# Optimization experiments

Measured on AMD Instinct MI355X. Metric: run time of the kernel, lower is better.

The kernel has to match this reference:

```python
import jax, jax.numpy as jnp
import numpy as np

B, T, C, J = 2048, 128, 3, 25   # batch, frames, coords, joints
E = 64                          # structure elements (n_elements)


def setup_inputs() -> dict:
    key = jax.random.key(0)
    k1, k2 = jax.random.split(key)
    x = jax.random.normal(k1, (B, T, C, J), dtype=jnp.float32)
    centres = jax.random.uniform(k2, (E, 2), dtype=jnp.float32)
    sharpness = jnp.full((E, 2), 3.0, dtype=jnp.float32)  # torch init: ones*3
    return {"x": x, "centres": centres, "sharpness": sharpness}


def _mst_deaths(Dm):
    """Prim's MST over dense distance matrix Dm [n,n].
    The multiset of MST edge weights equals the finite death times of the
    0-dim Vietoris-Rips persistence diagram (births are all 0)."""
    n = Dm.shape[0]
    in_tree0 = jnp.zeros(n, dtype=bool).at[0].set(True)

    def step(carry, _):
        mind, in_tree = carry
        masked = jnp.where(in_tree, jnp.inf, mind)  # distance from tree to each node
        j = jnp.argmin(masked)
        w = masked[j]                               # weight of edge added to MST
        in_tree = in_tree.at[j].set(True)
        mind = jnp.minimum(mind, Dm[j])
        return (mind, in_tree), w

    (_, _), deaths = jax.lax.scan(step, (Dm[0], in_tree0), None, length=n - 1)
    return deaths  # [n-1]


def reference(x, centres, sharpness):
    # --- dense preprocessing ---
    h = x.mean(1)                           # [B, C, J]
    h = h[..., :, None] - h[..., None, :]   # [B, C, J, J] pairwise coord diffs
    h = h.mean(-3)                          # [B, J, J]
    h = jnp.sqrt((h * h).sum(axis=1))       # torch.norm(., 2, dim=1) -> [B, J]
    lo, hi = h.min(), h.max()
    rng = hi - lo
    safe = rng > 1e-8
    h = jnp.where(safe, (h - lo) / jnp.where(safe, rng, 1.0), jnp.zeros_like(h))

    # --- Vietoris-Rips dim-0 persistence on point cloud h: B points in J dims ---
    sq = (h * h).sum(-1)
    d2 = sq[:, None] + sq[None, :] - 2.0 * (h @ h.T)       # [B, B]
    Dm = jnp.sqrt(jnp.maximum(d2, 1e-12))
    deaths = _mst_deaths(Dm)                               # [B-1]
    pd = jnp.stack([jnp.zeros_like(deaths), deaths], -1)[None]  # [1, P, 2]

    # --- StructureElementLayer: out[b,e] = sum_p exp(-sum_d s[e,d]^2 (pd-c)^2) ---
    s2 = sharpness * sharpness                             # [E, 2]
    diff = pd[:, :, None, :] - centres[None, None, :, :]   # [1, P, E, 2]
    out = jnp.exp(-(diff * diff * s2).sum(-1)).sum(1)      # [1, E]
    return out
```

## Files before the change

kernel.cpp:

```cpp
#include <hip/hip_runtime.h>
#include <math.h>

#define B_N 2048
#define T_N 128
#define C_N 3
#define J_N 25
#define E_N 64
#define TC  (T_N*C_N)
#define TCJ (TC*J_N)
#define NQ4 (TCJ/4)

#define D_OFF      0
#define H_OFF      (B_N*B_N)
#define BLO_OFF    (H_OFF + B_N*J_N)
#define BHI_OFF    (BLO_OFF + B_N)
#define DEATHS_OFF (BHI_OFF + B_N)
#define BEST_OFF   (DEATHS_OFF + B_N)
#define COMP_OFF   (BEST_OFF + 4*B_N)
#define GC_OFF     (COMP_OFF + 2*B_N)
#define DC_OFF     (GC_OFF + 2)

typedef unsigned long long u64;
#define U64MAX 0xFFFFFFFFFFFFFFFFull
#define U32INF 0xFFFFFFFFu

__global__ void __launch_bounds__(256) k_reduce(const float* __restrict__ x,
                                                float* __restrict__ ws) {
    __shared__ float4 part[250];
    __shared__ float S[100];
    __shared__ float Mj[25];
    const int t = threadIdx.x, b = blockIdx.x;
    const float4* x4 = (const float4*)(x + (size_t)b * TCJ);
    if (t < 250) {
        float4 a; a.x = a.y = a.z = a.w = 0.f;
        for (int idx = t; idx < NQ4; idx += 250) {
            float4 v = x4[idx];
            a.x += v.x; a.y += v.y; a.z += v.z; a.w += v.w;
        }
        part[t] = a;
    }
    __syncthreads();
    if (t < 25) {
        float4 s = part[t];
        #pragma unroll
        for (int g = 1; g < 10; ++g) {
            float4 v = part[t + 25 * g];
            s.x += v.x; s.y += v.y; s.z += v.z; s.w += v.w;
        }
        S[4*t] = s.x; S[4*t+1] = s.y; S[4*t+2] = s.z; S[4*t+3] = s.w;
    }
    __syncthreads();
    if (t < 25) Mj[t] = (S[t] + S[t+25] + S[t+50] + S[t+75]) * (1.0f / 384.0f);
    __syncthreads();
    if (t < 25) {
        float mj = Mj[t], acc = 0.f;
        #pragma unroll
        for (int i = 0; i < J_N; ++i) { float d = Mj[i] - mj; acc += d * d; }
        float hv = sqrtf(acc);
        ws[H_OFF + b * J_N + t] = hv;
        S[t] = hv;
    }
    __syncthreads();
    if (t == 0) {
        float lo = S[0], hi = S[0];
        #pragma unroll
        for (int i = 1; i < J_N; ++i) { lo = fminf(lo, S[i]); hi = fmaxf(hi, S[i]); }
        ws[BLO_OFF + b] = lo;
        ws[BHI_OFF + b] = hi;
    }
}

__global__ void k_dist(float* ws) {
    __shared__ float A[16][26], Bsh[16][26];
    const int tx = threadIdx.x, ty = threadIdx.y;
    const int flat = ty * 16 + tx;
    const int rowA = blockIdx.x * 16, rowB = blockIdx.y * 16;
    const float* h = ws + H_OFF;
    for (int idx = flat; idx < 16 * J_N; idx += 256) {
        int r = idx / J_N, c = idx % J_N;
        A[r][c]   = h[(rowA + r) * J_N + c];
        Bsh[r][c] = h[(rowB + r) * J_N + c];
    }
    __syncthreads();
    float acc = 0.f;
    #pragma unroll
    for (int k = 0; k < J_N; ++k) {
        float d = A[ty][k] - Bsh[tx][k];
        acc += d * d;
    }
    float* D = ws + D_OFF;
    D[(size_t)(rowA + ty) * B_N + rowB + tx] = sqrtf(fmaxf(acc, 1e-12f));
}

__global__ void __launch_bounds__(1024) k_scan0(float* __restrict__ ws) {
    const int t = threadIdx.x, w = t >> 6, lane = t & 63;
    const int row = blockIdx.x * 16 + w;
    const float4* row4 = (const float4*)(ws + D_OFF + (size_t)row * B_N);
    u64 best = U64MAX;
    #pragma unroll
    for (int k = 0; k < 8; ++k) {
        const int q = k * 64 + lane;
        float4 w4 = row4[q];
        const unsigned j0 = (unsigned)(q * 4);
        float wv[4] = {w4.x, w4.y, w4.z, w4.w};
        #pragma unroll
        for (int m = 0; m < 4; ++m) {
            unsigned j = j0 + m;
            if (j != (unsigned)row) {
                unsigned a = min((unsigned)row, j), b2 = max((unsigned)row, j);
                u64 key = ((u64)__float_as_uint(wv[m]) << 32) | (a << 11) | b2;
                if (key < best) best = key;
            }
        }
    }
    #pragma unroll
    for (int off = 32; off; off >>= 1) {
        u64 o = __shfl_down(best, off);
        if (o < best) best = o;
    }
    if (lane == 0) ((u64*)(ws + BEST_OFF))[row] = best;
    if (blockIdx.x == 0) {
        unsigned* gc = (unsigned*)(ws + COMP_OFF);
        gc[t] = (unsigned)t; gc[t + 1024] = (unsigned)(t + 1024);
        unsigned* dc = (unsigned*)(ws + DC_OFF);
        #pragma unroll
        for (int i = 0; i < 4; ++i) dc[i * 1024 + t] = U32INF;
        if (t == 0) { ((unsigned*)(ws + GC_OFF))[0] = 0u; ((unsigned*)(ws + GC_OFF))[1] = 0u; }
    }
}

__global__ void __launch_bounds__(1024) k_round(float* __restrict__ ws, int par_in,
                                                int do_scan) {
    unsigned* gcnt = (unsigned*)(ws + GC_OFF);
    const unsigned base = gcnt[par_in];
    if (base >= B_N - 1) return;
    __shared__ __align__(16) unsigned comp[B_N];
    __shared__ u64 cb[B_N];
    __shared__ unsigned par[B_N];
    __shared__ unsigned cnt_s;
    const int t = threadIdx.x, blk = blockIdx.x;
    const unsigned* gcomp_in = (const unsigned*)(ws + COMP_OFF) + par_in * B_N;
    unsigned* gcomp_out = (unsigned*)(ws + COMP_OFF) + (par_in ^ 1) * B_N;
    const u64* bin = (const u64*)(ws + BEST_OFF) + par_in * B_N;
    u64* bout = (u64*)(ws + BEST_OFF) + (par_in ^ 1) * B_N;
    float* deaths = ws + DEATHS_OFF;

    if (t == 0) cnt_s = 0u;
    comp[t] = gcomp_in[t]; comp[t + 1024] = gcomp_in[t + 1024];
    cb[t] = U64MAX; cb[t + 1024] = U64MAX;
    __syncthreads();
    #pragma unroll
    for (int i = t; i < B_N; i += 1024) {
        u64 bk = bin[i];
        if (bk != U64MAX) atomicMin(&cb[comp[i]], bk);
    }
    __syncthreads();
    #pragma unroll
    for (int c = t; c < B_N; c += 1024) {
        u64 k = cb[c];
        unsigned p = (unsigned)c;
        if (k != U64MAX) {
            unsigned a  = (unsigned)((k >> 11) & 0x7FFu);
            unsigned b2 = (unsigned)(k & 0x7FFu);
            unsigned ca = comp[a], cbv = comp[b2];
            unsigned c2 = (ca == (unsigned)c) ? cbv : ca;
            p = c2;
            if (!(cb[c2] == k && c2 < (unsigned)c)) {
                unsigned li = atomicAdd(&cnt_s, 1u);
                if (blk == 0) deaths[base + li] = __uint_as_float((unsigned)(k >> 32));
            }
        }
        par[c] = p;
    }
    __syncthreads();
    #pragma unroll
    for (int c = t; c < B_N; c += 1024) {
        unsigned p = par[c];
        if (p != (unsigned)c && par[p] == (unsigned)c && (unsigned)c < p) par[c] = (unsigned)c;
    }
    __syncthreads();
    #pragma unroll
    for (int c = t; c < B_N; c += 1024) {
        unsigned r = par[c];
        while (true) { unsigned pr = par[r]; if (pr == r) break; r = pr; }
        par[c] = r;
    }
    __syncthreads();
    #pragma unroll
    for (int i = t; i < B_N; i += 1024) comp[i] = par[comp[i]];
    __syncthreads();
    const unsigned newbase = base + cnt_s;
    if (blk == 0) {
        gcomp_out[t] = comp[t]; gcomp_out[t + 1024] = comp[t + 1024];
        if (t == 0) { gcnt[par_in ^ 1] = newbase; if (newbase >= B_N - 1) gcnt[par_in] = newbase; }
    }
    if (!do_scan || newbase >= B_N - 1) return;

    const int w = t >> 6, lane = t & 63;
    const int row = blk * 16 + w;
    const unsigned ci = comp[row];
    u64 prev = bin[row];
    {
        unsigned pa = (unsigned)((prev >> 11) & 0x7FFu);
        unsigned pb = (unsigned)(prev & 0x7FFu);
        unsigned jo = (pa == (unsigned)row) ? pb : pa;
        if (comp[jo] != ci) {
            if (lane == 0) bout[row] = prev;
            return;
        }
    }
    const float4* row4 = (const float4*)(ws + D_OFF + (size_t)row * B_N);
    const uint4* comp4 = (const uint4*)comp;
    u64 best = U64MAX;
    #pragma unroll
    for (int k = 0; k < 8; ++k) {
        const int q = k * 64 + lane;
        float4 w4 = row4[q];
        uint4  c4 = comp4[q];
        const unsigned j0 = (unsigned)(q * 4);
        float wv[4] = {w4.x, w4.y, w4.z, w4.w};
        unsigned cv[4] = {c4.x, c4.y, c4.z, c4.w};
        #pragma unroll
        for (int m = 0; m < 4; ++m) {
            if (cv[m] != ci) {
                unsigned j = j0 + m;
                unsigned a = min((unsigned)row, j), b2 = max((unsigned)row, j);
                u64 key = ((u64)__float_as_uint(wv[m]) << 32) | (a << 11) | b2;
                if (key < best) best = key;
            }
        }
    }
    #pragma unroll
    for (int off = 32; off; off >>= 1) {
        u64 o = __shfl_down(best, off);
        if (o < best) best = o;
    }
    if (lane == 0) bout[row] = best;
}

__global__ void __launch_bounds__(1024) k_contract(float* __restrict__ ws) {
    if (((const unsigned*)(ws + GC_OFF))[1] >= B_N - 1) return;
    __shared__ unsigned cflag[B_N];
    __shared__ unsigned Dcs[64 * 64];
    __shared__ unsigned csum[16];
    const int t = threadIdx.x, blk = blockIdx.x;
    const unsigned lane = t & 63, w = t >> 6;
    const unsigned* gcomp1 = (const unsigned*)(ws + COMP_OFF) + B_N;

    cflag[t] = 0u; cflag[t + 1024] = 0u;
    #pragma unroll
    for (int i = 0; i < 4; ++i) Dcs[i * 1024 + t] = U32INF;
    __syncthreads();
    unsigned cA = gcomp1[t], cB = gcomp1[t + 1024];
    cflag[cA] = 1u; cflag[cB] = 1u;
    __syncthreads();
    unsigned f0 = cflag[2 * t], f1 = cflag[2 * t + 1];
    unsigned s = f0 + f1, sc = s;
    #pragma unroll
    for (int off = 1; off < 64; off <<= 1) {
        unsigned v = __shfl_up(sc, off);
        if (lane >= (unsigned)off) sc += v;
    }
    if (lane == 63) csum[w] = sc;
    __syncthreads();
    if (t < 16) {
        unsigned v = csum[t], acc = v;
        #pragma unroll
        for (int off = 1; off < 16; off <<= 1) {
            unsigned u2 = __shfl_up(acc, off);
            if (t >= off) acc += u2;
        }
        csum[t] = acc - v;
    }
    __syncthreads();
    unsigned off0 = csum[w] + (sc - s);
    __syncthreads();
    if (f0) cflag[2 * t] = off0;
    if (f1) cflag[2 * t + 1] = off0 + f0;
    __syncthreads();

    #pragma unroll
    for (int q2 = 0; q2 < 2; ++q2) {
        const int row = blk * 32 + (int)w * 2 + q2;
        const unsigned ci = gcomp1[row];
        const unsigned ri = cflag[ci];
        const float4* row4 = (const float4*)(ws + D_OFF + (size_t)row * B_N);
        const uint4* comp4 = (const uint4*)gcomp1;
        #pragma unroll
        for (int k = 0; k < 8; ++k) {
            const int q = k * 64 + (int)lane;
            float4 w4 = row4[q];
            uint4  c4 = comp4[q];
            float wv[4] = {w4.x, w4.y, w4.z, w4.w};
            unsigned cv[4] = {c4.x, c4.y, c4.z, c4.w};
            #pragma unroll
            for (int m = 0; m < 4; ++m) {
                if (cv[m] != ci) {
                    unsigned rj = cflag[cv[m]];
                    atomicMin(&Dcs[ri * 64 + rj], __float_as_uint(wv[m]));
                }
            }
        }
    }
    __syncthreads();
    unsigned* gDc = (unsigned*)(ws + DC_OFF);
    #pragma unroll
    for (int i = t; i < 4096; i += 1024) {
        unsigned v = Dcs[i];
        if (v != U32INF) atomicMin(&gDc[i], v);
    }
}

__global__ void __launch_bounds__(1024) k_finishstruct(float* __restrict__ ws,
                                                       const float* __restrict__ centres,
                                                       const float* __restrict__ sharp,
                                                       float* __restrict__ out) {
    __shared__ unsigned Dcs[64 * 64];
    __shared__ u64 cbf[64];
    __shared__ unsigned parf[64], ccomp[64];
    __shared__ unsigned cnt_s, base_s;
    __shared__ float redlo[16], redhi[16];
    const int t = threadIdx.x;
    const unsigned lane = t & 63, w = t >> 6;
    float* deaths = ws + DEATHS_OFF;
    const unsigned base0 = ((const unsigned*)(ws + GC_OFF))[1];

    if (base0 < B_N - 1) {
        const unsigned* gDc = (const unsigned*)(ws + DC_OFF);
        #pragma unroll
        for (int i = 0; i < 4; ++i) Dcs[i * 1024 + t] = gDc[i * 1024 + t];
        if (t < 64) ccomp[t] = (unsigned)t;
        if (t == 0) base_s = base0;
        __syncthreads();
        for (int iter = 0; iter < 7; ++iter) {
            if (t < 64) cbf[t] = U64MAX;
            if (t == 0) cnt_s = 0u;
            __syncthreads();
            #pragma unroll
            for (int q2 = 0; q2 < 4; ++q2) {
                const int r = (int)w * 4 + q2;
                const unsigned cc = ccomp[r];
                unsigned wv = Dcs[r * 64 + lane];
                u64 key = U64MAX;
                if (wv != U32INF && ccomp[lane] != cc) {
                    unsigned a = min((unsigned)r, lane), b2 = max((unsigned)r, lane);
                    key = ((u64)wv << 32) | (a << 6) | b2;
                }
                #pragma unroll
                for (int off = 32; off; off >>= 1) {
                    u64 o = __shfl_down(key, off);
                    if (o < key) key = o;
                }
                if (lane == 0 && key != U64MAX) atomicMin(&cbf[cc], key);
            }
            __syncthreads();
            if (w == 0) {
                u64 k = cbf[lane];
                unsigned p = lane;
                bool add = false; float dw = 0.f;
                if (k != U64MAX) {
                    unsigned a = (unsigned)((k >> 6) & 63u), b2 = (unsigned)(k & 63u);
                    unsigned ca = ccomp[a], cbv = ccomp[b2];
                    unsigned c2 = (ca == lane) ? cbv : ca;
                    p = c2;
                    if (!(cbf[c2] == k && c2 < lane)) {
                        add = true; dw = __uint_as_float((unsigned)(k >> 32));
                    }
                }
                parf[lane] = p;
                unsigned pp = parf[lane];
                if (pp != lane && parf[pp] == lane && lane < pp) parf[lane] = lane;
                unsigned r2 = parf[lane];
                while (parf[r2] != r2) r2 = parf[r2];
                parf[lane] = r2;
                if (add) {
                    unsigned li = atomicAdd(&cnt_s, 1u);
                    deaths[base_s + li] = dw;
                }
                ccomp[lane] = parf[ccomp[lane]];
            }
            __syncthreads();
            if (t == 0) base_s += cnt_s;
            __syncthreads();
            if (base_s >= B_N - 1) break;
        }
        __threadfence_block();
        __syncthreads();
    }

    float lo = INFINITY, hi = -INFINITY;
    #pragma unroll
    for (int i = t; i < B_N; i += 1024) {
        lo = fminf(lo, ws[BLO_OFF + i]);
        hi = fmaxf(hi, ws[BHI_OFF + i]);
    }
    #pragma unroll
    for (int off = 32; off; off >>= 1) {
        lo = fminf(lo, __shfl_down(lo, off));
        hi = fmaxf(hi, __shfl_down(hi, off));
    }
    if (lane == 0) { redlo[w] = lo; redhi[w] = hi; }
    __syncthreads();
    lo = redlo[0]; hi = redhi[0];
    #pragma unroll
    for (int k = 1; k < 16; ++k) { lo = fminf(lo, redlo[k]); hi = fmaxf(hi, redhi[k]); }
    float rng = hi - lo;
    float rinv = (rng > 1e-8f) ? 1.0f / rng : 0.0f;

    for (int e = (int)w; e < E_N; e += 16) {
        const float c0 = centres[e * 2], c1 = centres[e * 2 + 1];
        const float s0 = sharp[e * 2],   s1 = sharp[e * 2 + 1];
        const float s1sq = s1 * s1;
        float acc = 0.f;
        for (int p = (int)lane; p < B_N - 1; p += 64) {
            float d = deaths[p] * rinv - c1;
            acc += expf(-s1sq * d * d);
        }
        #pragma unroll
        for (int off = 32; off; off >>= 1) acc += __shfl_down(acc, off);
        if (lane == 0) out[e] = expf(-s0 * s0 * c0 * c0) * acc;
    }
}

extern "C" void kernel_launch(void* const* d_in, const int* in_sizes, int n_in,
                              void* d_out, int out_size, void* d_ws, size_t ws_size,
                              hipStream_t stream) {
    const float* x       = (const float*)d_in[0];
    const float* centres = (const float*)d_in[1];
    const float* sharp   = (const float*)d_in[2];
    float* out = (float*)d_out;
    float* ws  = (float*)d_ws;

    hipLaunchKernelGGL(k_reduce,   dim3(B_N),      dim3(256),    0, stream, x, ws);
    hipLaunchKernelGGL(k_dist,     dim3(128, 128), dim3(16, 16), 0, stream, ws);
    hipLaunchKernelGGL(k_scan0,    dim3(128),      dim3(1024),   0, stream, ws);
    hipLaunchKernelGGL(k_round,    dim3(128),      dim3(1024),   0, stream, ws, 0, 1);
    hipLaunchKernelGGL(k_round,    dim3(128),      dim3(1024),   0, stream, ws, 1, 1);
    hipLaunchKernelGGL(k_round,    dim3(128),      dim3(1024),   0, stream, ws, 0, 1);
    hipLaunchKernelGGL(k_round,    dim3(128),      dim3(1024),   0, stream, ws, 1, 1);
    hipLaunchKernelGGL(k_round,    dim3(128),      dim3(1024),   0, stream, ws, 0, 0);
    hipLaunchKernelGGL(k_contract, dim3(64),       dim3(1024),   0, stream, ws);
    hipLaunchKernelGGL(k_finishstruct, dim3(1),    dim3(1024),   0, stream, ws, centres, sharp, out);
}
```

Baseline: 187.3 us.

## Fuse final Boruvka round with contraction, widen contracted graph, retile distance kernel

The pipeline of Boruvka rounds is restructured. There are now three scan rounds, and the old fourth and fifth rounds are fused with contraction into one kernel (k_round4c), which removes a launch and a full pass. The contracted component graph grows from 64 to 128 nodes, so the single-block finishing kernel handles a larger dense matrix with more barriers. The distance kernel now uses 32x32 tiles with 4 outputs per thread for more reuse of the shared-memory tiles. The risk is that the finish stage becomes heavier and shared memory per block in the fused kernel is large.

```diff
diff --git a/kernel.cpp b/kernel.cpp
--- a/kernel.cpp
+++ b/kernel.cpp
@@ -9,6 +9,7 @@
 #define TC  (T_N*C_N)
 #define TCJ (TC*J_N)
 #define NQ4 (TCJ/4)
+#define NC  128
 
 #define D_OFF      0
 #define H_OFF      (B_N*B_N)
@@ -70,26 +71,30 @@
     }
 }
 
-__global__ void k_dist(float* ws) {
-    __shared__ float A[16][26], Bsh[16][26];
-    const int tx = threadIdx.x, ty = threadIdx.y;
-    const int flat = ty * 16 + tx;
-    const int rowA = blockIdx.x * 16, rowB = blockIdx.y * 16;
+__global__ void __launch_bounds__(256) k_dist(float* ws) {
+    __shared__ float A[32][27], Bsh[32][27];
+    const int t = threadIdx.x;
+    const int rowA = blockIdx.x * 32, rowB = blockIdx.y * 32;
     const float* h = ws + H_OFF;
-    for (int idx = flat; idx < 16 * J_N; idx += 256) {
+    for (int idx = t; idx < 32 * J_N; idx += 256) {
         int r = idx / J_N, c = idx % J_N;
         A[r][c]   = h[(rowA + r) * J_N + c];
         Bsh[r][c] = h[(rowB + r) * J_N + c];
     }
     __syncthreads();
-    float acc = 0.f;
-    #pragma unroll
-    for (int k = 0; k < J_N; ++k) {
-        float d = A[ty][k] - Bsh[tx][k];
-        acc += d * d;
-    }
+    const int tx = t & 31, ty = t >> 5;
     float* D = ws + D_OFF;
-    D[(size_t)(rowA + ty) * B_N + rowB + tx] = sqrtf(fmaxf(acc, 1e-12f));
+    #pragma unroll
+    for (int rr = 0; rr < 4; ++rr) {
+        const int r = ty + rr * 8;
+        float acc = 0.f;
+        #pragma unroll
+        for (int k = 0; k < J_N; ++k) {
+            float d = A[r][k] - Bsh[tx][k];
+            acc += d * d;
+        }
+        D[(size_t)(rowA + r) * B_N + rowB + tx] = sqrtf(fmaxf(acc, 1e-12f));
+    }
 }
 
 __global__ void __launch_bounds__(1024) k_scan0(float* __restrict__ ws) {
@@ -119,18 +124,15 @@
         if (o < best) best = o;
     }
     if (lane == 0) ((u64*)(ws + BEST_OFF))[row] = best;
+    if (blockIdx.x < 16) ((unsigned*)(ws + DC_OFF))[blockIdx.x * 1024 + t] = U32INF;
     if (blockIdx.x == 0) {
         unsigned* gc = (unsigned*)(ws + COMP_OFF);
         gc[t] = (unsigned)t; gc[t + 1024] = (unsigned)(t + 1024);
-        unsigned* dc = (unsigned*)(ws + DC_OFF);
-        #pragma unroll
-        for (int i = 0; i < 4; ++i) dc[i * 1024 + t] = U32INF;
         if (t == 0) { ((unsigned*)(ws + GC_OFF))[0] = 0u; ((unsigned*)(ws + GC_OFF))[1] = 0u; }
     }
 }
 
-__global__ void __launch_bounds__(1024) k_round(float* __restrict__ ws, int par_in,
-                                                int do_scan) {
+__global__ void __launch_bounds__(1024) k_round(float* __restrict__ ws, int par_in) {
     unsigned* gcnt = (unsigned*)(ws + GC_OFF);
     const unsigned base = gcnt[par_in];
     if (base >= B_N - 1) return;
@@ -194,7 +196,7 @@
         gcomp_out[t] = comp[t]; gcomp_out[t + 1024] = comp[t + 1024];
         if (t == 0) { gcnt[par_in ^ 1] = newbase; if (newbase >= B_N - 1) gcnt[par_in] = newbase; }
     }
-    if (!do_scan || newbase >= B_N - 1) return;
+    if (newbase >= B_N - 1) return;
 
     const int w = t >> 6, lane = t & 63;
     const int row = blk * 16 + w;
@@ -238,22 +240,74 @@
     if (lane == 0) bout[row] = best;
 }
 
-__global__ void __launch_bounds__(1024) k_contract(float* __restrict__ ws) {
-    if (((const unsigned*)(ws + GC_OFF))[1] >= B_N - 1) return;
+__global__ void __launch_bounds__(1024) k_round4c(float* __restrict__ ws) {
+    unsigned* gcnt = (unsigned*)(ws + GC_OFF);
+    const unsigned base = gcnt[1];
+    if (base >= B_N - 1) return;
+    __shared__ __align__(16) unsigned comp[B_N];
+    __shared__ __align__(16) unsigned ovl[NC*NC];
     __shared__ unsigned cflag[B_N];
-    __shared__ unsigned Dcs[64 * 64];
-    __shared__ unsigned csum[16];
+    __shared__ unsigned cnt_s, csum[16];
+    u64* cb = (u64*)ovl;
+    unsigned* par = ovl + 4096;
     const int t = threadIdx.x, blk = blockIdx.x;
+    const unsigned* gcomp_in = (const unsigned*)(ws + COMP_OFF) + B_N;
+    const u64* bin = (const u64*)(ws + BEST_OFF) + B_N;
+    float* deaths = ws + DEATHS_OFF;
+
+    if (t == 0) cnt_s = 0u;
+    comp[t] = gcomp_in[t]; comp[t + 1024] = gcomp_in[t + 1024];
+    cb[t] = U64MAX; cb[t + 1024] = U64MAX;
+    __syncthreads();
+    #pragma unroll
+    for (int i = t; i < B_N; i += 1024) {
+        u64 bk = bin[i];
+        if (bk != U64MAX) atomicMin(&cb[comp[i]], bk);
+    }
+    __syncthreads();
+    #pragma unroll
+    for (int c = t; c < B_N; c += 1024) {
+        u64 k = cb[c];
+        unsigned p = (unsigned)c;
+        if (k != U64MAX) {
+            unsigned a  = (unsigned)((k >> 11) & 0x7FFu);
+            unsigned b2 = (unsigned)(k & 0x7FFu);
+            unsigned ca = comp[a], cbv = comp[b2];
+            unsigned c2 = (ca == (unsigned)c) ? cbv : ca;
+            p = c2;
+            if (!(cb[c2] == k && c2 < (unsigned)c)) {
+                unsigned li = atomicAdd(&cnt_s, 1u);
+                if (blk == 0) deaths[base + li] = __uint_as_float((unsigned)(k >> 32));
+            }
+        }
+        par[c] = p;
+    }
+    __syncthreads();
+    #pragma unroll
+    for (int c = t; c < B_N; c += 1024) {
+        unsigned p = par[c];
+        if (p != (unsigned)c && par[p] == (unsigned)c && (unsigned)c < p) par[c] = (unsigned)c;
+    }
+    __syncthreads();
+    #pragma unroll
+    for (int c = t; c < B_N; c += 1024) {
+        unsigned r = par[c];
+        while (true) { unsigned pr = par[r]; if (pr == r) break; r = pr; }
+        par[c] = r;
+    }
+    __syncthreads();
+    #pragma unroll
+    for (int i = t; i < B_N; i += 1024) comp[i] = par[comp[i]];
+    __syncthreads();
+    const unsigned newbase = base + cnt_s;
+    if (blk == 0 && t == 0) { gcnt[0] = newbase; gcnt[1] = newbase; }
+    if (newbase >= B_N - 1) return;
+
+    cflag[t] = 0u; cflag[t + 1024] = 0u;
+    __syncthreads();
+    cflag[comp[t]] = 1u; cflag[comp[t + 1024]] = 1u;
+    __syncthreads();
     const unsigned lane = t & 63, w = t >> 6;
-    const unsigned* gcomp1 = (const unsigned*)(ws + COMP_OFF) + B_N;
-
-    cflag[t] = 0u; cflag[t + 1024] = 0u;
-    #pragma unroll
-    for (int i = 0; i < 4; ++i) Dcs[i * 1024 + t] = U32INF;
-    __syncthreads();
-    unsigned cA = gcomp1[t], cB = gcomp1[t + 1024];
-    cflag[cA] = 1u; cflag[cB] = 1u;
-    __syncthreads();
     unsigned f0 = cflag[2 * t], f1 = cflag[2 * t + 1];
     unsigned s = f0 + f1, sc = s;
     #pragma unroll
@@ -280,12 +334,14 @@
     __syncthreads();
 
     #pragma unroll
-    for (int q2 = 0; q2 < 2; ++q2) {
-        const int row = blk * 32 + (int)w * 2 + q2;
-        const unsigned ci = gcomp1[row];
+    for (int i = 0; i < 16; ++i) ovl[i * 1024 + t] = U32INF;
+    __syncthreads();
+    {
+        const int row = blk * 16 + (int)w;
+        const unsigned ci = comp[row];
         const unsigned ri = cflag[ci];
         const float4* row4 = (const float4*)(ws + D_OFF + (size_t)row * B_N);
-        const uint4* comp4 = (const uint4*)gcomp1;
+        const uint4* comp4 = (const uint4*)comp;
         #pragma unroll
         for (int k = 0; k < 8; ++k) {
             const int q = k * 64 + (int)lane;
@@ -295,18 +351,15 @@
             unsigned cv[4] = {c4.x, c4.y, c4.z, c4.w};
             #pragma unroll
             for (int m = 0; m < 4; ++m) {
-                if (cv[m] != ci) {
-                    unsigned rj = cflag[cv[m]];
-                    atomicMin(&Dcs[ri * 64 + rj], __float_as_uint(wv[m]));
-                }
+                if (cv[m] != ci) atomicMin(&ovl[ri * NC + cflag[cv[m]]], __float_as_uint(wv[m]));
             }
         }
     }
     __syncthreads();
     unsigned* gDc = (unsigned*)(ws + DC_OFF);
     #pragma unroll
-    for (int i = t; i < 4096; i += 1024) {
-        unsigned v = Dcs[i];
+    for (int i = t; i < NC * NC; i += 1024) {
+        unsigned v = ovl[i];
         if (v != U32INF) atomicMin(&gDc[i], v);
     }
 }
@@ -315,36 +368,42 @@
                                                        const float* __restrict__ centres,
                                                        const float* __restrict__ sharp,
                                                        float* __restrict__ out) {
-    __shared__ unsigned Dcs[64 * 64];
-    __shared__ u64 cbf[64];
-    __shared__ unsigned parf[64], ccomp[64];
+    __shared__ unsigned Dcs[NC * NC];
+    __shared__ u64 cbf[NC];
+    __shared__ unsigned parf[NC], ccomp[NC];
     __shared__ unsigned cnt_s, base_s;
     __shared__ float redlo[16], redhi[16];
     const int t = threadIdx.x;
-    const unsigned lane = t & 63, w = t >> 6;
+    const int lane = t & 63, w = t >> 6;
     float* deaths = ws + DEATHS_OFF;
-    const unsigned base0 = ((const unsigned*)(ws + GC_OFF))[1];
+    const unsigned base0 = ((const unsigned*)(ws + GC_OFF))[0];
 
     if (base0 < B_N - 1) {
         const unsigned* gDc = (const unsigned*)(ws + DC_OFF);
         #pragma unroll
-        for (int i = 0; i < 4; ++i) Dcs[i * 1024 + t] = gDc[i * 1024 + t];
-        if (t < 64) ccomp[t] = (unsigned)t;
+        for (int i = 0; i < 16; ++i) Dcs[i * 1024 + t] = gDc[i * 1024 + t];
+        if (t < NC) ccomp[t] = (unsigned)t;
         if (t == 0) base_s = base0;
         __syncthreads();
         for (int iter = 0; iter < 7; ++iter) {
-            if (t < 64) cbf[t] = U64MAX;
+            if (t < NC) cbf[t] = U64MAX;
             if (t == 0) cnt_s = 0u;
             __syncthreads();
             #pragma unroll
-            for (int q2 = 0; q2 < 4; ++q2) {
-                const int r = (int)w * 4 + q2;
+            for (int q = 0; q < 8; ++q) {
+                const int r = w * 8 + q;
                 const unsigned cc = ccomp[r];
-                unsigned wv = Dcs[r * 64 + lane];
                 u64 key = U64MAX;
-                if (wv != U32INF && ccomp[lane] != cc) {
-                    unsigned a = min((unsigned)r, lane), b2 = max((unsigned)r, lane);
-                    key = ((u64)wv << 32) | (a << 6) | b2;
+                #pragma unroll
+                for (int hh = 0; hh < 2; ++hh) {
+                    const int c = lane + hh * 64;
+                    unsigned wv = Dcs[r * NC + c];
+                    if (wv != U32INF && ccomp[c] != cc) {
+                        unsigned a = min((unsigned)r, (unsigned)c);
+                        unsigned b2 = max((unsigned)r, (unsigned)c);
+                        u64 k2 = ((u64)wv << 32) | (a << 7) | b2;
+                        if (k2 < key) key = k2;
+                    }
                 }
                 #pragma unroll
                 for (int off = 32; off; off >>= 1) {
@@ -354,30 +413,36 @@
                 if (lane == 0 && key != U64MAX) atomicMin(&cbf[cc], key);
             }
             __syncthreads();
-            if (w == 0) {
-                u64 k = cbf[lane];
-                unsigned p = lane;
-                bool add = false; float dw = 0.f;
+            bool add = false; float dw = 0.f;
+            if (t < NC) {
+                u64 k = cbf[t];
+                unsigned p = (unsigned)t;
                 if (k != U64MAX) {
-                    unsigned a = (unsigned)((k >> 6) & 63u), b2 = (unsigned)(k & 63u);
+                    unsigned a = (unsigned)((k >> 7) & 127u), b2 = (unsigned)(k & 127u);
                     unsigned ca = ccomp[a], cbv = ccomp[b2];
-                    unsigned c2 = (ca == lane) ? cbv : ca;
+                    unsigned c2 = (ca == (unsigned)t) ? cbv : ca;
                     p = c2;
-                    if (!(cbf[c2] == k && c2 < lane)) {
+                    if (!(cbf[c2] == k && c2 < (unsigned)t)) {
                         add = true; dw = __uint_as_float((unsigned)(k >> 32));
                     }
                 }
-                parf[lane] = p;
-                unsigned pp = parf[lane];
-                if (pp != lane && parf[pp] == lane && lane < pp) parf[lane] = lane;
-                unsigned r2 = parf[lane];
+                parf[t] = p;
+            }
+            __syncthreads();
+            if (t < NC) {
+                unsigned pp = parf[t];
+                if (pp != (unsigned)t && parf[pp] == (unsigned)t && (unsigned)t < pp) parf[t] = (unsigned)t;
+            }
+            __syncthreads();
+            if (t < NC) {
+                unsigned r2 = parf[t];
                 while (parf[r2] != r2) r2 = parf[r2];
-                parf[lane] = r2;
-                if (add) {
-                    unsigned li = atomicAdd(&cnt_s, 1u);
-                    deaths[base_s + li] = dw;
-                }
-                ccomp[lane] = parf[ccomp[lane]];
+                parf[t] = r2;
+            }
+            __syncthreads();
+            if (t < NC) {
+                if (add) { unsigned li = atomicAdd(&cnt_s, 1u); deaths[base_s + li] = dw; }
+                ccomp[t] = parf[ccomp[t]];
             }
             __syncthreads();
             if (t == 0) base_s += cnt_s;
@@ -407,12 +472,12 @@
     float rng = hi - lo;
     float rinv = (rng > 1e-8f) ? 1.0f / rng : 0.0f;
 
-    for (int e = (int)w; e < E_N; e += 16) {
+    for (int e = w; e < E_N; e += 16) {
         const float c0 = centres[e * 2], c1 = centres[e * 2 + 1];
         const float s0 = sharp[e * 2],   s1 = sharp[e * 2 + 1];
         const float s1sq = s1 * s1;
         float acc = 0.f;
-        for (int p = (int)lane; p < B_N - 1; p += 64) {
+        for (int p = lane; p < B_N - 1; p += 64) {
             float d = deaths[p] * rinv - c1;
             acc += expf(-s1sq * d * d);
         }
@@ -431,14 +496,12 @@
     float* out = (float*)d_out;
     float* ws  = (float*)d_ws;
 
-    hipLaunchKernelGGL(k_reduce,   dim3(B_N),      dim3(256),    0, stream, x, ws);
-    hipLaunchKernelGGL(k_dist,     dim3(128, 128), dim3(16, 16), 0, stream, ws);
-    hipLaunchKernelGGL(k_scan0,    dim3(128),      dim3(1024),   0, stream, ws);
-    hipLaunchKernelGGL(k_round,    dim3(128),      dim3(1024),   0, stream, ws, 0, 1);
-    hipLaunchKernelGGL(k_round,    dim3(128),      dim3(1024),   0, stream, ws, 1, 1);
-    hipLaunchKernelGGL(k_round,    dim3(128),      dim3(1024),   0, stream, ws, 0, 1);
-    hipLaunchKernelGGL(k_round,    dim3(128),      dim3(1024),   0, stream, ws, 1, 1);
-    hipLaunchKernelGGL(k_round,    dim3(128),      dim3(1024),   0, stream, ws, 0, 0);
-    hipLaunchKernelGGL(k_contract, dim3(64),       dim3(1024),   0, stream, ws);
-    hipLaunchKernelGGL(k_finishstruct, dim3(1),    dim3(1024),   0, stream, ws, centres, sharp, out);
-}
+    hipLaunchKernelGGL(k_reduce,   dim3(B_N),    dim3(256),  0, stream, x, ws);
+    hipLaunchKernelGGL(k_dist,     dim3(64, 64), dim3(256),  0, stream, ws);
+    hipLaunchKernelGGL(k_scan0,    dim3(128),    dim3(1024), 0, stream, ws);
+    hipLaunchKernelGGL(k_round,    dim3(128),    dim3(1024), 0, stream, ws, 0);
+    hipLaunchKernelGGL(k_round,    dim3(128),    dim3(1024), 0, stream, ws, 1);
+    hipLaunchKernelGGL(k_round,    dim3(128),    dim3(1024), 0, stream, ws, 0);
+    hipLaunchKernelGGL(k_round4c,  dim3(128),    dim3(1024), 0, stream, ws);
+    hipLaunchKernelGGL(k_finishstruct, dim3(1),  dim3(1024), 0, stream, ws, centres, sharp, out);
+}
```

New measurement: 186.8 us. About the same (-0.3%).
